# Kernel tuning notes

Measured on AMD Instinct MI355X. Metric: run time of the kernel, lower is better.

## Reference

```python
import jax, jax.numpy as jnp
import numpy as np

D_MODEL = 512
NUM_HEADS = 8
D_HEAD = D_MODEL // NUM_HEADS


def setup_inputs() -> dict:
    key = jax.random.key(0)
    ks = jax.random.split(key, 16)
    B, S, D, H, dh = 8, 1024, D_MODEL, NUM_HEADS, D_HEAD
    s = 1.0 / np.sqrt(D)
    return {
        "query": jax.random.normal(ks[0], (B, S, D), jnp.float32),
        "key": jax.random.normal(ks[1], (B, S, D), jnp.float32),
        "value": jax.random.normal(ks[2], (B, S, D), jnp.float32),
        "pos_emb": jax.random.normal(ks[3], (B, S, D), jnp.float32),
        "Wq": jax.random.normal(ks[4], (D, D), jnp.float32) * s,
        "bq": jnp.zeros((D,), jnp.float32),
        "Wk": jax.random.normal(ks[5], (D, D), jnp.float32) * s,
        "bk": jnp.zeros((D,), jnp.float32),
        "Wv": jax.random.normal(ks[6], (D, D), jnp.float32) * s,
        "bv": jnp.zeros((D,), jnp.float32),
        "Wpos": jax.random.normal(ks[7], (D, D), jnp.float32) * s,  # pos_proj has no bias
        "Wo": jax.random.normal(ks[8], (D, D), jnp.float32) * s,
        "bo": jnp.zeros((D,), jnp.float32),
        "u_bias": jax.random.normal(ks[9], (H, dh), jnp.float32) * 0.02,
        "v_bias": jax.random.normal(ks[10], (H, dh), jnp.float32) * 0.02,
    }


def _rel_shift(x):
    # x: [B, H, S, S] -> Transformer-XL relative shift
    B, H, S1, S2 = x.shape
    x = jnp.pad(x, ((0, 0), (0, 0), (0, 0), (1, 0)))  # zero col at front
    x = x.reshape(B, H, S2 + 1, S1)[:, :, 1:, :]
    return x.reshape(B, H, S1, S2)


def reference(query, key, value, pos_emb, Wq, bq, Wk, bk, Wv, bv, Wpos, Wo, bo, u_bias, v_bias):
    B, S, D = query.shape
    H, dh = NUM_HEADS, D_HEAD
    q = (query @ Wq + bq).reshape(B, S, H, dh)      # [B,S,H,dh]
    k = (key @ Wk + bk).reshape(B, S, H, dh)
    v = (value @ Wv + bv).reshape(B, S, H, dh)
    p = (pos_emb @ Wpos).reshape(B, S, H, dh)
    content_score = jnp.einsum('bqhd,bkhd->bhqk', q + u_bias, k)
    pos_score = _rel_shift(jnp.einsum('bqhd,bkhd->bhqk', q + v_bias, p))
    score = (content_score + pos_score) / jnp.sqrt(jnp.float32(D))
    attn = jax.nn.softmax(score, axis=-1)
    ctx = jnp.einsum('bhqk,bkhd->bqhd', attn, v).reshape(B, S, D)
    return ctx @ Wo + bo
```

## Files before the change

kernel.cpp:

```cpp
#include <hip/hip_runtime.h>
#include <hip/hip_bf16.h>

typedef unsigned short u16;
typedef unsigned int u32;
typedef __attribute__((ext_vector_type(4))) float f32x4;
typedef __attribute__((ext_vector_type(8))) short s16x8;
typedef __attribute__((ext_vector_type(4))) short s16x4;

#define DEV static __device__ __forceinline__

DEV u16 f2bf(float f){ return __builtin_bit_cast(u16, __float2bfloat16(f)); }
DEV float bf2f(u16 v){ union{u32 u;float f;}x; x.u = ((u32)v)<<16; return x.f; }
DEV float bitsf(u32 u){ union{u32 u;float f;}x; x.u = u; return x.f; }

DEV f32x4 MF(s16x8 a, s16x8 b, f32x4 c){ return __builtin_amdgcn_mfma_f32_16x16x32_bf16(a,b,c,0,0,0); }

DEV s16x8 frag64(const u16* lds, int row, int slot){
  return *(const s16x8*)(lds + row*64 + ((slot ^ (row&7))<<3));
}

__global__ __launch_bounds__(256) void k_prep(
  const float* __restrict__ Wq, const float* __restrict__ Wk, const float* __restrict__ Wv,
  const float* __restrict__ Wp, const float* __restrict__ Wo, u16* __restrict__ WT)
{
  const int bx = blockIdx.x; const int mat = bx>>6, tile = bx&63;
  const float* W = (mat==0)?Wq:(mat==1)?Wk:(mat==2)?Wv:(mat==3)?Wp:Wo;
  u16* dst = WT + mat*262144;
  const int k0 = (tile>>3)<<6, n0 = (tile&7)<<6;
  __shared__ u16 L[64*68];
  const int t = threadIdx.x;
#pragma unroll
  for (int i=0;i<4;i++){
    int id = t + 256*i; int row = id>>4, c4 = (id&15)<<2;
    float4 v = *(const float4*)(W + (k0+row)*512 + n0 + c4);
    s16x4 o; o[0]=(short)f2bf(v.x); o[1]=(short)f2bf(v.y); o[2]=(short)f2bf(v.z); o[3]=(short)f2bf(v.w);
    *(s16x4*)(L + row*68 + c4) = o;
  }
  __syncthreads();
#pragma unroll
  for (int i=0;i<2;i++){
    int id = t + 256*i; int nl = id>>3, slot = id&7;
    s16x8 v;
#pragma unroll
    for (int j=0;j<8;j++) v[j] = (short)L[(slot*8+j)*68 + nl];
    *(s16x8*)(dst + (n0+nl)*512 + k0 + slot*8) = v;
  }
}

__global__ __launch_bounds__(256,2) void k_proj(
  const float* __restrict__ Xq, const float* __restrict__ Xk,
  const float* __restrict__ Xv, const float* __restrict__ Xp,
  const u16* __restrict__ WT,
  const float* __restrict__ bq, const float* __restrict__ bk, const float* __restrict__ bv,
  const float* __restrict__ ub, const float* __restrict__ vb,
  u16* __restrict__ Qu, u16* __restrict__ Qv, u16* __restrict__ Kb,
  u16* __restrict__ Pb, u16* __restrict__ Vt)
{
  const int Lb = blockIdx.x;
  const int xcd = Lb & 7, li = Lb >> 3;
  const int n0  = (li & 3) * 128;
  const int job = (li >> 2) & 3;
  const int m0  = (xcd*8 + (li >> 4)) * 128;
  const float* X = (job==0)?Xq:(job==1)?Xk:(job==2)?Xp:Xv;
  const int wsel = (job==0)?0:(job==1)?1:(job==2)?3:2;
  const u16* W = WT + wsel*262144;
  __shared__ u16 As[128*64];
  __shared__ u16 Bs[128*64];
  const int t = threadIdx.x, lane = t&63, w = t>>6;
  const int wm = w&1, wn = w>>1;
  f32x4 acc[4][4];
#pragma unroll
  for (int i=0;i<4;i++)
#pragma unroll
    for (int j=0;j<4;j++) acc[i][j] = (f32x4){0.f,0.f,0.f,0.f};

  for (int kt=0; kt<8; ++kt){
    const int k0 = kt*64;
    __syncthreads();
#pragma unroll
    for (int i=0;i<8;i++){
      int id = t + 256*i; int row = id>>4; int c4 = (id&15)<<2;
      float4 v = *(const float4*)(X + (m0+row)*512 + k0 + c4);
      s16x4 o; o[0]=(short)f2bf(v.x); o[1]=(short)f2bf(v.y); o[2]=(short)f2bf(v.z); o[3]=(short)f2bf(v.w);
      *(s16x4*)(As + row*64 + ((((c4>>3)^(row&7))<<3) + (c4&4))) = o;
    }
#pragma unroll
    for (int i=0;i<4;i++){
      int id = t + 256*i; int row = id>>3, slot = id&7;
      s16x8 v = *(const s16x8*)(W + (n0+row)*512 + k0 + slot*8);
      *(s16x8*)(Bs + row*64 + ((slot^(row&7))<<3)) = v;
    }
    __syncthreads();
#pragma unroll
    for (int kk=0;kk<2;kk++){
      const int slotk = kk*4 + (lane>>4);
      s16x8 xf[4], wf[4];
#pragma unroll
      for (int j=0;j<4;j++){ int r = wm*64 + j*16 + (lane&15); xf[j] = frag64(As, r, slotk); }
#pragma unroll
      for (int i=0;i<4;i++){ int r = wn*64 + i*16 + (lane&15); wf[i] = frag64(Bs, r, slotk); }
      if (job != 3){
#pragma unroll
        for (int i=0;i<4;i++)
#pragma unroll
          for (int j=0;j<4;j++) acc[i][j] = MF(wf[i], xf[j], acc[i][j]);
      } else {
#pragma unroll
        for (int i=0;i<4;i++)
#pragma unroll
          for (int j=0;j<4;j++) acc[i][j] = MF(xf[i], wf[j], acc[i][j]);
      }
    }
  }

  const int b = m0>>10;
  if (job != 3){
#pragma unroll
    for (int i=0;i<4;i++){
      const int n = n0 + wn*64 + i*16 + ((lane>>4)<<2);
      const int hh = n>>6, d = n&63;
      f32x4 b1 = {0.f,0.f,0.f,0.f}, b2 = {0.f,0.f,0.f,0.f};
      if (job==0){
        f32x4 q4 = *(const f32x4*)(bq+n); f32x4 u4 = *(const f32x4*)(ub+n); f32x4 v4 = *(const f32x4*)(vb+n);
        b1 = q4 + u4; b2 = q4 + v4;
      } else if (job==1){
        b1 = *(const f32x4*)(bk+n);
      }
#pragma unroll
      for (int j=0;j<4;j++){
        const int m = m0 + wm*64 + j*16 + (lane&15);
        const int s = m&1023;
        const int off = ((b*8+hh)*1024 + s)*64 + d;
        f32x4 a = acc[i][j];
        s16x4 o1;
#pragma unroll
        for (int r=0;r<4;r++) o1[r] = (short)f2bf(a[r]+b1[r]);
        if (job==0){
          *(s16x4*)(Qu+off) = o1;
          s16x4 o2;
#pragma unroll
          for (int r=0;r<4;r++) o2[r] = (short)f2bf(a[r]+b2[r]);
          *(s16x4*)(Qv+off) = o2;
        } else if (job==1) *(s16x4*)(Kb+off) = o1;
        else               *(s16x4*)(Pb+off) = o1;
      }
    }
  } else {
#pragma unroll
    for (int j=0;j<4;j++){
      const int n = n0 + wn*64 + j*16 + (lane&15);
      const int hh = n>>6, d = n&63;
      const float bvn = bv[n];
#pragma unroll
      for (int i=0;i<4;i++){
        const int m = m0 + wm*64 + i*16 + ((lane>>4)<<2);
        const int s = m&1023;
        f32x4 a = acc[i][j];
        s16x4 o;
#pragma unroll
        for (int r=0;r<4;r++) o[r] = (short)f2bf(a[r]+bvn);
        *(s16x4*)(Vt + ((b*8+hh)*64 + d)*1024 + s) = o;
      }
    }
  }
}

#define SC_SLOT(q, slot) ((((slot)) & ~7) | ((((slot))&7) ^ ((q)&7)))

__global__ __launch_bounds__(512,2) void k_attn(
  const u16* __restrict__ Qu, const u16* __restrict__ Qv,
  const u16* __restrict__ Kb, const u16* __restrict__ Pb,
  const u16* __restrict__ Vt, u16* __restrict__ Ctx)
{
  const int Lb = blockIdx.x;
  const int xcd = Lb & 7, li = Lb >> 3;
  const int bh = xcd*8 + (li>>5);
  const int qb = li & 31;
  const int q0 = qb*32;
  const u16* Qu_ = Qu + bh*65536;
  const u16* Qv_ = Qv + bh*65536;
  const u16* Kb_ = Kb + bh*65536;
  const u16* Pb_ = Pb + bh*65536;
  const u16* Vt_ = Vt + bh*65536;
  u16* Ctx_ = Ctx + bh*65536;
  __shared__ u16 sc[33*1024];
  __shared__ u16 Ts[4096];
  __shared__ float pmax[512];
  __shared__ float stats[32];
  const int t = threadIdx.x, lane = t&63, w = t>>6;
  const int l15 = lane&15, lg = lane>>4;
  const int qband = w&1, sub = w>>1;
  const int qi = qband*16 + l15;
  const int q  = q0 + qi;
  const int srow = t>>3, sslot = t&7;
  u16* tsw = Ts + srow*64 + ((sslot^(srow&7))<<3);
  const u16* srcP = Pb_ + srow*64 + sslot*8;
  const u16* srcK = Kb_ + srow*64 + sslot*8;
  const u16* srcV = Vt_ + srow*1024 + sslot*8;

  s16x8 p0 = *(const s16x8*)(srcP);
  s16x8 p1 = *(const s16x8*)(srcP + 4096);

  const int priBand = w>>2, jtp = w&3;
  s16x8 qvp[2], qvb2[2];
#pragma unroll
  for (int kk=0;kk<2;kk++){
    qvp[kk]  = *(const s16x8*)(Qv_ + (q0 + priBand*16 + l15)*64 + (kk*4+lg)*8);
    int r2 = q0 + 17 + l15; if (r2 > 1023) r2 = 1023;
    qvb2[kk] = *(const s16x8*)(Qv_ + r2*64 + (kk*4+lg)*8);
  }

  {
#pragma unroll
    for (int u=0; u<16; ++u){
      __syncthreads();
      *(s16x8*)tsw = p0;
      p0 = p1;
      if (u+2<16) p1 = *(const s16x8*)(srcP + (u+2)*4096);
      __syncthreads();
      {
        f32x4 ps = {0.f,0.f,0.f,0.f};
#pragma unroll
        for (int kk=0;kk<2;kk++){
          s16x8 pf = frag64(Ts, jtp*16 + l15, kk*4+lg);
          ps = MF(pf, qvp[kk], ps);
        }
        const int prow = priBand*16 + l15;
        const int j0 = u*64 + jtp*16 + lg*4;
        s16x4 o;
#pragma unroll
        for (int r=0;r<4;r++) o[r] = (short)f2bf(ps[r]);
        *(s16x4*)(sc + prow*1024 + ((((j0>>2) ^ ((prow&15)<<1)))<<2)) = o;
      }
      if ((u&1) == (w>>2)){
        f32x4 ps = {0.f,0.f,0.f,0.f};
#pragma unroll
        for (int kk=0;kk<2;kk++){
          s16x8 pf = frag64(Ts, (w&3)*16 + l15, kk*4+lg);
          ps = MF(pf, qvb2[kk], ps);
        }
        if (l15 == 15){
          const int j0 = u*64 + (w&3)*16 + lg*4;
          s16x4 o;
#pragma unroll
          for (int r=0;r<4;r++) o[r] = (short)f2bf(ps[r]);
          *(s16x4*)(sc + 32*1024 + ((j0>>2)<<2)) = o;
        }
      }
    }
  }

  __syncthreads();

  s16x8 qfu[2];
#pragma unroll
  for (int kk=0;kk<2;kk++)
    qfu[kk] = *(const s16x8*)(Qu_ + q*64 + (kk*4+lg)*8);
  s16x8 k0r = *(const s16x8*)(srcK);
  s16x8 k1r = *(const s16x8*)(srcK + 4096);

  u32 stash[32];
#pragma unroll
  for (int kt=0; kt<16; ++kt){
#pragma unroll
    for (int rp=0; rp<2; ++rp){
      u32 wv = 0;
#pragma unroll
      for (int hh=0; hh<2; ++hh){
        const int k = kt*64 + sub*16 + lg*4 + rp*2 + hh;
        const int above = (k > q) ? 1 : 0;
        int jj = above ? (k - q - 2) : (1023 - q + k);
        const bool zero = (k == q+1);
        if (jj < 0) jj = 0;
        const int row = qi + above;
        const int addr = row*1024 + ((((jj>>2) ^ ((row&15)<<1)))<<2) + (jj&3);
        u32 v = zero ? 0u : (u32)sc[addr];
        wv |= v << (16*hh);
      }
      stash[kt*2+rp] = wv;
    }
  }

  float rmax = -1e30f;
  {
#pragma unroll
    for (int kt=0; kt<16; ++kt){
      __syncthreads();
      *(s16x8*)tsw = k0r;
      k0r = k1r;
      if (kt+2<16) k1r = *(const s16x8*)(srcK + (kt+2)*4096);
      __syncthreads();
      f32x4 a = {0.f,0.f,0.f,0.f};
#pragma unroll
      for (int kk=0;kk<2;kk++){
        s16x8 kf = frag64(Ts, sub*16 + l15, kk*4+lg);
        a = MF(kf, qfu[kk], a);
      }
      const int kb2 = kt*64 + sub*16 + lg*4;
      const u32 w0 = stash[kt*2], w1 = stash[kt*2+1];
      const float v0 = a[0] + bitsf(w0<<16);
      const float v1 = a[1] + bitsf(w0 & 0xffff0000u);
      const float v2 = a[2] + bitsf(w1<<16);
      const float v3 = a[3] + bitsf(w1 & 0xffff0000u);
      rmax = fmaxf(rmax, fmaxf(fmaxf(v0,v1), fmaxf(v2,v3)));
      s16x4 o;
      o[0]=(short)f2bf(v0); o[1]=(short)f2bf(v1);
      o[2]=(short)f2bf(v2); o[3]=(short)f2bf(v3);
      *(s16x4*)(sc + qi*1024 + SC_SLOT(qi, kb2>>3)*8 + (kb2&4)) = o;
    }
  }
  pmax[qi*16 + sub*4 + lg] = rmax;

  __syncthreads();

  s16x8 v0r = *(const s16x8*)(srcV);
  s16x8 v1r = *(const s16x8*)(srcV + 64);

  {
    const int row = t>>4, c = t&15;
    float mx = pmax[row*16 + c];
    mx = fmaxf(mx, __shfl_xor(mx,1));
    mx = fmaxf(mx, __shfl_xor(mx,2));
    mx = fmaxf(mx, __shfl_xor(mx,4));
    mx = fmaxf(mx, __shfl_xor(mx,8));
    const float S2 = 0.063762029f;
    const float nm = -mx * S2;
    float sum = 0.f;
#pragma unroll
    for (int i=0;i<8;i++){
      const int slot = c + 16*i;
      u16* p = sc + row*1024 + SC_SLOT(row,slot)*8;
      s16x8 v = *(const s16x8*)p;
      s16x8 o;
#pragma unroll
      for (int j2=0;j2<8;j2++){
        float e = exp2f(__builtin_fmaf(bf2f((u16)v[j2]), S2, nm));
        sum += e; o[j2] = (short)f2bf(e);
      }
      *(s16x8*)p = o;
    }
    sum += __shfl_xor(sum,1); sum += __shfl_xor(sum,2);
    sum += __shfl_xor(sum,4); sum += __shfl_xor(sum,8);
    if (c==0) stats[row] = 1.0f/sum;
  }

  f32x4 accC = {0.f,0.f,0.f,0.f};
  const int dtile = w>>1;
  {
#pragma unroll
    for (int kt=0; kt<16; ++kt){
      __syncthreads();
      *(s16x8*)tsw = v0r;
      v0r = v1r;
      if (kt+2<16) v1r = *(const s16x8*)(srcV + (kt+2)*64);
      __syncthreads();
#pragma unroll
      for (int kk=0;kk<2;kk++){
        const int slotk = kk*4 + lg;
        s16x8 vf = frag64(Ts, dtile*16 + l15, slotk);
        const int slot = kt*8 + slotk;
        s16x8 pfr = *(const s16x8*)(sc + qi*1024 + SC_SLOT(qi,slot)*8);
        accC = MF(vf, pfr, accC);
      }
    }
  }
  {
    const float inv = stats[qi];
    const int d0 = dtile*16 + lg*4;
    s16x4 o;
#pragma unroll
    for (int r=0;r<4;r++) o[r] = (short)f2bf(accC[r]*inv);
    *(s16x4*)(Ctx_ + (q0+qi)*64 + d0) = o;
  }
}

__global__ __launch_bounds__(256,2) void k_out(
  const u16* __restrict__ Ctx, const u16* __restrict__ WT,
  const float* __restrict__ bo, float* __restrict__ Out)
{
  const u16* W = WT + 4*262144;
  const int m0 = blockIdx.y*128, n0 = blockIdx.x*128;
  const int b = m0>>10, s0 = m0&1023;
  __shared__ u16 As[128*64];
  __shared__ u16 Bs[128*64];
  const int t = threadIdx.x, lane = t&63, w = t>>6;
  const int wm = w&1, wn = w>>1;
  f32x4 acc[4][4];
#pragma unroll
  for (int i=0;i<4;i++)
#pragma unroll
    for (int j=0;j<4;j++) acc[i][j] = (f32x4){0.f,0.f,0.f,0.f};

  for (int kt=0; kt<8; ++kt){
    const int k0 = kt*64, hh = kt;
    __syncthreads();
#pragma unroll
    for (int i=0;i<4;i++){
      int id = t + 256*i; int row = id>>3, slot = id&7;
      s16x8 v = *(const s16x8*)(Ctx + ((b*8+hh)*1024 + s0 + row)*64 + slot*8);
      *(s16x8*)(As + row*64 + ((slot^(row&7))<<3)) = v;
    }
#pragma unroll
    for (int i=0;i<4;i++){
      int id = t + 256*i; int row = id>>3, slot = id&7;
      s16x8 v = *(const s16x8*)(W + (n0+row)*512 + k0 + slot*8);
      *(s16x8*)(Bs + row*64 + ((slot^(row&7))<<3)) = v;
    }
    __syncthreads();
#pragma unroll
    for (int kk=0;kk<2;kk++){
      const int slotk = kk*4 + (lane>>4);
      s16x8 xf[4], wf[4];
#pragma unroll
      for (int j=0;j<4;j++){ int r = wm*64 + j*16 + (lane&15); xf[j] = frag64(As, r, slotk); }
#pragma unroll
      for (int i=0;i<4;i++){ int r = wn*64 + i*16 + (lane&15); wf[i] = frag64(Bs, r, slotk); }
#pragma unroll
      for (int i=0;i<4;i++)
#pragma unroll
        for (int j=0;j<4;j++) acc[i][j] = MF(wf[i], xf[j], acc[i][j]);
    }
  }
#pragma unroll
  for (int i=0;i<4;i++){
    const int n = n0 + wn*64 + i*16 + ((lane>>4)<<2);
    f32x4 bo4 = *(const f32x4*)(bo + n);
#pragma unroll
    for (int j=0;j<4;j++){
      const int m = m0 + wm*64 + j*16 + (lane&15);
      f32x4 o = acc[i][j] + bo4;
      *(f32x4*)(Out + m*512 + n) = o;
    }
  }
}

extern "C" void kernel_launch(void* const* d_in, const int* in_sizes, int n_in,
                              void* d_out, int out_size, void* d_ws, size_t ws_size,
                              hipStream_t stream)
{
  const float* query = (const float*)d_in[0];
  const float* key   = (const float*)d_in[1];
  const float* value = (const float*)d_in[2];
  const float* pos   = (const float*)d_in[3];
  const float* Wq = (const float*)d_in[4];
  const float* bq = (const float*)d_in[5];
  const float* Wk = (const float*)d_in[6];
  const float* bk = (const float*)d_in[7];
  const float* Wv = (const float*)d_in[8];
  const float* bv = (const float*)d_in[9];
  const float* Wp = (const float*)d_in[10];
  const float* Wo = (const float*)d_in[11];
  const float* bo = (const float*)d_in[12];
  const float* ub = (const float*)d_in[13];
  const float* vb = (const float*)d_in[14];
  float* Out = (float*)d_out;

  u16* ws  = (u16*)d_ws;
  u16* WT  = ws;
  u16* Qu  = ws + 1310720;
  u16* Qv  = Qu + 4194304;
  u16* Kb  = Qv + 4194304;
  u16* Pb  = Kb + 4194304;
  u16* Vt  = Pb + 4194304;
  u16* Ctx = Vt + 4194304;

  k_prep<<<dim3(320),  dim3(256), 0, stream>>>(Wq,Wk,Wv,Wp,Wo,WT);
  k_proj<<<dim3(1024), dim3(256), 0, stream>>>(query,key,value,pos,WT,bq,bk,bv,ub,vb,Qu,Qv,Kb,Pb,Vt);
  k_attn<<<dim3(2048), dim3(512), 0, stream>>>(Qu,Qv,Kb,Pb,Vt,Ctx);
  k_out<<<dim3(4,64),  dim3(256), 0, stream>>>(Ctx,WT,bo,Out);
}
```

Measured before the change: 175.7 us.

## Give each wave a private LDS tile to drop per-iteration block barriers

Each wave now stages its own 16-row slice of P, K and V into a private LDS region, so the two __syncthreads per inner iteration in all three loops go away. The extra pos-score row (33rd) is folded into row 0 with wraparound indexing, which shrinks LDS usage. Row-max and sum statistics move into the per-wave scratch, replacing the separate pmax and stats arrays. The cost is that each wave issues twice as many global loads per step, and the row-0 aliasing needs careful index bounds.

Result: slower. 226.5 us (+28.9%).

```diff
diff --git a/kernel.cpp b/kernel.cpp
--- a/kernel.cpp
+++ b/kernel.cpp
@@ -183,25 +183,30 @@
   const u16* Pb_ = Pb + bh*65536;
   const u16* Vt_ = Vt + bh*65536;
   u16* Ctx_ = Ctx + bh*65536;
-  __shared__ u16 sc[33*1024];
-  __shared__ u16 Ts[4096];
-  __shared__ float pmax[512];
-  __shared__ float stats[32];
+  __shared__ u16 sc[32*1024];
+  __shared__ u16 Ts[8*1024];
   const int t = threadIdx.x, lane = t&63, w = t>>6;
   const int l15 = lane&15, lg = lane>>4;
   const int qband = w&1, sub = w>>1;
   const int qi = qband*16 + l15;
   const int q  = q0 + qi;
-  const int srow = t>>3, sslot = t&7;
-  u16* tsw = Ts + srow*64 + ((sslot^(srow&7))<<3);
-  const u16* srcP = Pb_ + srow*64 + sslot*8;
-  const u16* srcK = Kb_ + srow*64 + sslot*8;
-  const u16* srcV = Vt_ + srow*1024 + sslot*8;
-
-  s16x8 p0 = *(const s16x8*)(srcP);
-  s16x8 p1 = *(const s16x8*)(srcP + 4096);
-
+  u16* myTs = Ts + w*1024;
+  float* myTsF = (float*)myTs;
+
+  const int srowL = lane>>2;
+  const int ssl0  = (lane&3)<<1;
+  u16* tw0 = myTs + srowL*64 + (((ssl0  )^(srowL&7))<<3);
+  u16* tw1 = myTs + srowL*64 + (((ssl0+1)^(srowL&7))<<3);
   const int priBand = w>>2, jtp = w&3;
+  const u16* gP = Pb_ + (jtp*16 + srowL)*64 + ssl0*8;
+  const u16* gK = Kb_ + (sub*16 + srowL)*64 + ssl0*8;
+  const u16* gV = Vt_ + (sub*16 + srowL)*1024 + ssl0*8;
+
+  s16x8 pa0 = *(const s16x8*)(gP);
+  s16x8 pa1 = *(const s16x8*)(gP + 8);
+  s16x8 pb0 = *(const s16x8*)(gP + 4096);
+  s16x8 pb1 = *(const s16x8*)(gP + 4096 + 8);
+
   s16x8 qvp[2], qvb2[2];
 #pragma unroll
   for (int kk=0;kk<2;kk++){
@@ -213,38 +218,49 @@
   {
 #pragma unroll
     for (int u=0; u<16; ++u){
-      __syncthreads();
-      *(s16x8*)tsw = p0;
-      p0 = p1;
-      if (u+2<16) p1 = *(const s16x8*)(srcP + (u+2)*4096);
-      __syncthreads();
+      *(s16x8*)tw0 = pa0;
+      *(s16x8*)tw1 = pa1;
+      pa0 = pb0; pa1 = pb1;
+      if (u+2<16){
+        pb0 = *(const s16x8*)(gP + (u+2)*4096);
+        pb1 = *(const s16x8*)(gP + (u+2)*4096 + 8);
+      }
       {
         f32x4 ps = {0.f,0.f,0.f,0.f};
 #pragma unroll
         for (int kk=0;kk<2;kk++){
-          s16x8 pf = frag64(Ts, jtp*16 + l15, kk*4+lg);
+          s16x8 pf = frag64(myTs, l15, kk*4+lg);
           ps = MF(pf, qvp[kk], ps);
         }
         const int prow = priBand*16 + l15;
         const int j0 = u*64 + jtp*16 + lg*4;
-        s16x4 o;
-#pragma unroll
-        for (int r=0;r<4;r++) o[r] = (short)f2bf(ps[r]);
-        *(s16x4*)(sc + prow*1024 + ((((j0>>2) ^ ((prow&15)<<1)))<<2)) = o;
+        if (prow){
+          s16x4 o;
+#pragma unroll
+          for (int r=0;r<4;r++) o[r] = (short)f2bf(ps[r]);
+          *(s16x4*)(sc + prow*1024 + ((((j0>>2) ^ ((prow&15)<<1)))<<2)) = o;
+        } else {
+#pragma unroll
+          for (int r=0;r<4;r++){
+            const int jj = j0 + r;
+            if (jj >= 1023 - q0) sc[jj] = f2bf(ps[r]);
+          }
+        }
       }
       if ((u&1) == (w>>2)){
         f32x4 ps = {0.f,0.f,0.f,0.f};
 #pragma unroll
         for (int kk=0;kk<2;kk++){
-          s16x8 pf = frag64(Ts, (w&3)*16 + l15, kk*4+lg);
+          s16x8 pf = frag64(myTs, l15, kk*4+lg);
           ps = MF(pf, qvb2[kk], ps);
         }
         if (l15 == 15){
           const int j0 = u*64 + (w&3)*16 + lg*4;
-          s16x4 o;
-#pragma unroll
-          for (int r=0;r<4;r++) o[r] = (short)f2bf(ps[r]);
-          *(s16x4*)(sc + 32*1024 + ((j0>>2)<<2)) = o;
+#pragma unroll
+          for (int r=0;r<4;r++){
+            const int jj = j0 + r;
+            if (jj <= 990 - q0) sc[jj] = f2bf(ps[r]);
+          }
         }
       }
     }
@@ -256,8 +272,10 @@
 #pragma unroll
   for (int kk=0;kk<2;kk++)
     qfu[kk] = *(const s16x8*)(Qu_ + q*64 + (kk*4+lg)*8);
-  s16x8 k0r = *(const s16x8*)(srcK);
-  s16x8 k1r = *(const s16x8*)(srcK + 4096);
+  s16x8 ka0 = *(const s16x8*)(gK);
+  s16x8 ka1 = *(const s16x8*)(gK + 8);
+  s16x8 kb0 = *(const s16x8*)(gK + 4096);
+  s16x8 kb1 = *(const s16x8*)(gK + 4096 + 8);
 
   u32 stash[32];
 #pragma unroll
@@ -272,8 +290,8 @@
         int jj = above ? (k - q - 2) : (1023 - q + k);
         const bool zero = (k == q+1);
         if (jj < 0) jj = 0;
-        const int row = qi + above;
-        const int addr = row*1024 + ((((jj>>2) ^ ((row&15)<<1)))<<2) + (jj&3);
+        const int phys = (qi + above) & 31;
+        const int addr = phys*1024 + ((((jj>>2) ^ ((phys&15)<<1)))<<2) + (jj&3);
         u32 v = zero ? 0u : (u32)sc[addr];
         wv |= v << (16*hh);
       }
@@ -281,19 +299,23 @@
     }
   }
 
+  __syncthreads();
+
   float rmax = -1e30f;
   {
 #pragma unroll
     for (int kt=0; kt<16; ++kt){
-      __syncthreads();
-      *(s16x8*)tsw = k0r;
-      k0r = k1r;
-      if (kt+2<16) k1r = *(const s16x8*)(srcK + (kt+2)*4096);
-      __syncthreads();
+      *(s16x8*)tw0 = ka0;
+      *(s16x8*)tw1 = ka1;
+      ka0 = kb0; ka1 = kb1;
+      if (kt+2<16){
+        kb0 = *(const s16x8*)(gK + (kt+2)*4096);
+        kb1 = *(const s16x8*)(gK + (kt+2)*4096 + 8);
+      }
       f32x4 a = {0.f,0.f,0.f,0.f};
 #pragma unroll
       for (int kk=0;kk<2;kk++){
-        s16x8 kf = frag64(Ts, sub*16 + l15, kk*4+lg);
+        s16x8 kf = frag64(myTs, l15, kk*4+lg);
         a = MF(kf, qfu[kk], a);
       }
       const int kb2 = kt*64 + sub*16 + lg*4;
@@ -309,20 +331,24 @@
       *(s16x4*)(sc + qi*1024 + SC_SLOT(qi, kb2>>3)*8 + (kb2&4)) = o;
     }
   }
-  pmax[qi*16 + sub*4 + lg] = rmax;
+  rmax = fmaxf(rmax, __shfl_xor(rmax,16));
+  rmax = fmaxf(rmax, __shfl_xor(rmax,32));
+  if (lane < 16) myTsF[l15] = rmax;
 
   __syncthreads();
 
-  s16x8 v0r = *(const s16x8*)(srcV);
-  s16x8 v1r = *(const s16x8*)(srcV + 64);
+  s16x8 va0 = *(const s16x8*)(gV);
+  s16x8 va1 = *(const s16x8*)(gV + 8);
+  s16x8 vb0 = *(const s16x8*)(gV + 64);
+  s16x8 vb1 = *(const s16x8*)(gV + 64 + 8);
 
   {
     const int row = t>>4, c = t&15;
-    float mx = pmax[row*16 + c];
-    mx = fmaxf(mx, __shfl_xor(mx,1));
-    mx = fmaxf(mx, __shfl_xor(mx,2));
-    mx = fmaxf(mx, __shfl_xor(mx,4));
-    mx = fmaxf(mx, __shfl_xor(mx,8));
+    const int qbR = row>>4, rl = row&15;
+    float mx =            ((const float*)(Ts + (qbR  )*1024))[rl];
+    mx = fmaxf(mx, ((const float*)(Ts + (qbR+2)*1024))[rl]);
+    mx = fmaxf(mx, ((const float*)(Ts + (qbR+4)*1024))[rl]);
+    mx = fmaxf(mx, ((const float*)(Ts + (qbR+6)*1024))[rl]);
     const float S2 = 0.063762029f;
     const float nm = -mx * S2;
     float sum = 0.f;
@@ -341,23 +367,28 @@
     }
     sum += __shfl_xor(sum,1); sum += __shfl_xor(sum,2);
     sum += __shfl_xor(sum,4); sum += __shfl_xor(sum,8);
-    if (c==0) stats[row] = 1.0f/sum;
-  }
+    if (c==0) ((float*)(Ts + (t>>6)*1024))[16 + (row&3)] = 1.0f/sum;
+  }
+
+  __syncthreads();
+  const float inv = ((const float*)(Ts + (qi>>2)*1024))[16 + (qi&3)];
+  __syncthreads();
 
   f32x4 accC = {0.f,0.f,0.f,0.f};
-  const int dtile = w>>1;
   {
 #pragma unroll
     for (int kt=0; kt<16; ++kt){
-      __syncthreads();
-      *(s16x8*)tsw = v0r;
-      v0r = v1r;
-      if (kt+2<16) v1r = *(const s16x8*)(srcV + (kt+2)*64);
-      __syncthreads();
+      *(s16x8*)tw0 = va0;
+      *(s16x8*)tw1 = va1;
+      va0 = vb0; va1 = vb1;
+      if (kt+2<16){
+        vb0 = *(const s16x8*)(gV + (kt+2)*64);
+        vb1 = *(const s16x8*)(gV + (kt+2)*64 + 8);
+      }
 #pragma unroll
       for (int kk=0;kk<2;kk++){
         const int slotk = kk*4 + lg;
-        s16x8 vf = frag64(Ts, dtile*16 + l15, slotk);
+        s16x8 vf = frag64(myTs, l15, slotk);
         const int slot = kt*8 + slotk;
         s16x8 pfr = *(const s16x8*)(sc + qi*1024 + SC_SLOT(qi,slot)*8);
         accC = MF(vf, pfr, accC);
@@ -365,8 +396,7 @@
     }
   }
   {
-    const float inv = stats[qi];
-    const int d0 = dtile*16 + lg*4;
+    const int d0 = sub*16 + lg*4;
     s16x4 o;
 #pragma unroll
     for (int r=0;r<4;r++) o[r] = (short)f2bf(accC[r]*inv);
```
